# Optimization experiments

Hardware: AMD Instinct MI355X
Metric: run time of the kernel (lower is better)

## Reference

```python
import jax, jax.numpy as jnp
import numpy as np

N = 8192
D = 128
NUM_CLASSES = 1000
MARGIN = 1.0
EPS = 1e-6  # torch.nn.functional.pairwise_distance default eps
FMAX = float(np.finfo(np.float32).max)


def setup_inputs() -> dict:
    key = jax.random.key(0)
    k_e, k_l = jax.random.split(key)
    embed = jax.random.normal(k_e, (N, D), dtype=jnp.float32)
    labels = jax.random.randint(k_l, (N,), 0, NUM_CLASSES, dtype=jnp.int64)
    return {"embed": embed, "labels": labels}


def reference(embed, labels):
    # Pairwise squared-L2 distance matrix: ||xi||^2 - 2 xi.xj + ||xj||^2  -> [N, N]
    norm_sq = jnp.sum(embed * embed, axis=1, keepdims=True)  # [N, 1]
    dist = norm_sq - 2.0 * (embed @ embed.T) + norm_sq.T     # [N, N]

    # Label similarity mask (int in original; float here for the multiplies)
    sim = (labels[:, None] == labels[None, :]).astype(dist.dtype)  # [N, N]

    # Hardest positive: argmax of masked distances
    hardest_pos = jnp.argmax(dist * sim, axis=1)  # [N]

    # Hardest negative: argmin over negatives, sentinel-replacing masked-out entries
    neg_masked = dist * (1.0 - sim)
    hardest_neg = jnp.argmin(neg_masked + (neg_masked <= 0).astype(dist.dtype) * FMAX, axis=1)

    a = embed
    p = embed[hardest_pos]  # [N, D]
    n = embed[hardest_neg]  # [N, D]

    # torch.nn.TripletMarginLoss(margin=MARGIN): mean(relu(d(a,p) - d(a,n) + margin))
    # with d(x, y) = ||x - y + eps||_2 (torch pairwise_distance semantics)
    d_ap = jnp.sqrt(jnp.sum((a - p + EPS) ** 2, axis=1))
    d_an = jnp.sqrt(jnp.sum((a - n + EPS) ** 2, axis=1))
    loss = jnp.mean(jnp.maximum(d_ap - d_an + MARGIN, 0.0))
    return loss
```

## Files before the change

kernel.cpp:

```cpp
#include <hip/hip_runtime.h>
#include <cstdint>

typedef unsigned long long u64;
typedef _Float16 half8 __attribute__((ext_vector_type(8)));
typedef float f32x4 __attribute__((ext_vector_type(4)));

static constexpr int Dd = 128;
static constexpr float EPSf = 1e-6f;
static constexpr float MARGINf = 1.0f;
static constexpr float BIGf = 3.0e38f;

__device__ __forceinline__ unsigned fkey(float f) {
  unsigned b = __float_as_uint(f);
  return (b & 0x80000000u) ? ~b : (b | 0x80000000u);
}

__global__ __launch_bounds__(256) void k_prep(const float* __restrict__ E,
                                              _Float16* __restrict__ Ehp,
                                              float* __restrict__ normf) {
  __shared__ float part[4][16];
  const int t = threadIdx.x;
  const int b = blockIdx.x;
  const int ks = t >> 6, r15 = t & 15;
  const int lg = (t >> 4) & 3;
  const float* src = E + (size_t)(b * 16 + r15) * Dd + ks * 32 + lg * 8;
  float4 v0 = *(const float4*)src;
  float4 v1 = *(const float4*)(src + 4);
  half8 hv;
  hv[0] = (_Float16)v0.x; hv[1] = (_Float16)v0.y;
  hv[2] = (_Float16)v0.z; hv[3] = (_Float16)v0.w;
  hv[4] = (_Float16)v1.x; hv[5] = (_Float16)v1.y;
  hv[6] = (_Float16)v1.z; hv[7] = (_Float16)v1.w;
  *(half8*)((char*)Ehp + (size_t)b * 4096 + t * 16) = hv;
  float s = v0.x * v0.x + v0.y * v0.y + v0.z * v0.z + v0.w * v0.w +
            v1.x * v1.x + v1.y * v1.y + v1.z * v1.z + v1.w * v1.w;
  s += __shfl_xor(s, 16);
  s += __shfl_xor(s, 32);
  if (((t >> 4) & 3) == 0) part[ks][r15] = s;
  __syncthreads();
  if (t < 16) normf[b * 16 + t] = part[0][t] + part[1][t] + part[2][t] + part[3][t];
}

__global__ __launch_bounds__(256, 2) void k_gemm(const _Float16* __restrict__ Ehp,
                                                 const float* __restrict__ normf,
                                                 const int* __restrict__ lab,
                                                 u64* __restrict__ posPart,
                                                 u64* __restrict__ negPart) {
  __shared__ __align__(16) char Jb[2][32768];
  __shared__ __align__(16) float njs[1024];
  __shared__ __align__(16) int ljs[1024];

  const int t = threadIdx.x;
  const int w = t >> 6, l = t & 63;
  const int lane15 = l & 15, lg = l >> 4;
  const int iw = w & 1, jw = w >> 1;
  const int panel = blockIdx.x;
  const int strip = blockIdx.y;
  const int ibase = panel * 128;
  const int jbase = strip * 1024;
  const char* jsrc = (const char*)Ehp + (size_t)(jbase >> 4) * 4096;

  #pragma unroll
  for (int q = 0; q < 8; ++q)
    *(half8*)(Jb[0] + q * 4096 + t * 16) = *(const half8*)(jsrc + q * 4096 + t * 16);
  *(float4*)&njs[t * 4] = *(const float4*)&normf[jbase + t * 4];
  *(int4*)&ljs[t * 4] = *(const int4*)&lab[jbase + t * 4];

  const int gi0 = ibase + iw * 64;
  half8 bf[4][4];
  #pragma unroll
  for (int it = 0; it < 4; ++it)
    #pragma unroll
    for (int ks = 0; ks < 4; ++ks)
      bf[it][ks] = *(const half8*)(Ehp + ((size_t)((gi0 >> 4) + it) * 4 + ks) * 512 +
                                   (size_t)l * 8);
  int li[4];
  #pragma unroll
  for (int it = 0; it < 4; ++it) li[it] = lab[gi0 + it * 16 + lane15];
  __syncthreads();

  float bp[4] = {-BIGf, -BIGf, -BIGf, -BIGf};
  float bn[4] = {BIGf, BIGf, BIGf, BIGf};

  for (int tile = 0; tile < 8; ++tile) {
    const int cur = tile & 1;
    half8 sreg[8];
    if (tile < 7) {
      const char* s = jsrc + (size_t)(tile + 1) * 32768;
      #pragma unroll
      for (int q = 0; q < 8; ++q) sreg[q] = *(const half8*)(s + q * 4096 + t * 16);
    }

    f32x4 acc[4][4];
    #pragma unroll
    for (int a = 0; a < 4; ++a)
      #pragma unroll
      for (int b = 0; b < 4; ++b) acc[a][b] = (f32x4){0.f, 0.f, 0.f, 0.f};

    #pragma unroll
    for (int ks = 0; ks < 4; ++ks) {
      half8 aj[4];
      #pragma unroll
      for (int jt = 0; jt < 4; ++jt)
        aj[jt] = *(const half8*)(Jb[cur] + ((jw * 4 + jt) * 4 + ks) * 1024 + l * 16);
      __builtin_amdgcn_s_setprio(1);
      #pragma unroll
      for (int jt = 0; jt < 4; ++jt)
        #pragma unroll
        for (int it = 0; it < 4; ++it)
          acc[jt][it] = __builtin_amdgcn_mfma_f32_16x16x32_f16(aj[jt], bf[it][ks], acc[jt][it], 0, 0, 0);
      __builtin_amdgcn_s_setprio(0);
    }

    #pragma unroll
    for (int jt = 0; jt < 4; ++jt) {
      const int jr0 = tile * 128 + jw * 64 + jt * 16 + lg * 4;
      const float4 nj4 = *(const float4*)&njs[jr0];
      const int4 lj4 = *(const int4*)&ljs[jr0];
      #pragma unroll
      for (int it = 0; it < 4; ++it) {
        float c0 = fmaf(acc[jt][it][0], -2.0f, nj4.x);
        float c1 = fmaf(acc[jt][it][1], -2.0f, nj4.y);
        float c2 = fmaf(acc[jt][it][2], -2.0f, nj4.z);
        float c3 = fmaf(acc[jt][it][3], -2.0f, nj4.w);
        c0 = __uint_as_float((__float_as_uint(c0) & 0xFFFFFC00u) | (unsigned)(jr0 + 0));
        c1 = __uint_as_float((__float_as_uint(c1) & 0xFFFFFC00u) | (unsigned)(jr0 + 1));
        c2 = __uint_as_float((__float_as_uint(c2) & 0xFFFFFC00u) | (unsigned)(jr0 + 2));
        c3 = __uint_as_float((__float_as_uint(c3) & 0xFFFFFC00u) | (unsigned)(jr0 + 3));
        bool s0 = (lj4.x == li[it]), s1 = (lj4.y == li[it]);
        bool s2 = (lj4.z == li[it]), s3 = (lj4.w == li[it]);
        float p0 = s0 ? c0 : -BIGf, p1 = s1 ? c1 : -BIGf;
        float p2 = s2 ? c2 : -BIGf, p3 = s3 ? c3 : -BIGf;
        float n0 = s0 ? BIGf : c0, n1 = s1 ? BIGf : c1;
        float n2 = s2 ? BIGf : c2, n3 = s3 ? BIGf : c3;
        bp[it] = fmaxf(bp[it], fmaxf(fmaxf(p0, p1), fmaxf(p2, p3)));
        bn[it] = fminf(bn[it], fminf(fminf(n0, n1), fminf(n2, n3)));
      }
    }

    if (tile < 7) {
      #pragma unroll
      for (int q = 0; q < 8; ++q)
        *(half8*)(Jb[cur ^ 1] + q * 4096 + t * 16) = sreg[q];
    }
    __syncthreads();
  }

  #pragma unroll
  for (int it = 0; it < 4; ++it) {
    bp[it] = fmaxf(bp[it], __shfl_xor(bp[it], 16));
    bp[it] = fmaxf(bp[it], __shfl_xor(bp[it], 32));
    bn[it] = fminf(bn[it], __shfl_xor(bn[it], 16));
    bn[it] = fminf(bn[it], __shfl_xor(bn[it], 32));
  }
  if (l < 16) {
    const int slot = strip * 2 + jw;
    #pragma unroll
    for (int it = 0; it < 4; ++it) {
      int gi = ibase + iw * 64 + it * 16 + lane15;
      unsigned gjp = (unsigned)jbase + (__float_as_uint(bp[it]) & 1023u);
      unsigned gjn = (unsigned)jbase + (__float_as_uint(bn[it]) & 1023u);
      posPart[(size_t)slot * 8192 + gi] =
          ((u64)fkey(bp[it]) << 32) | (u64)(0xFFFFFFFFu - gjp);
      negPart[(size_t)slot * 8192 + gi] = ((u64)fkey(bn[it]) << 32) | (u64)gjn;
    }
  }
}

__global__ __launch_bounds__(256) void k_final(const float* __restrict__ E,
                                               const u64* __restrict__ posPart,
                                               const u64* __restrict__ negPart,
                                               float* __restrict__ rowLoss) {
  int i = (blockIdx.x * 256 + threadIdx.x) >> 6;
  int l = threadIdx.x & 63;
  u64 pp = 0ull, np = ~0ull;
  if (l < 16) {
    pp = posPart[(size_t)l * 8192 + i];
    np = negPart[(size_t)l * 8192 + i];
  }
  #pragma unroll
  for (int off = 1; off < 64; off <<= 1) {
    u64 a = __shfl_xor(pp, off);
    u64 b = __shfl_xor(np, off);
    pp = pp > a ? pp : a;
    np = np < b ? np : b;
  }
  int jp = (int)((0xFFFFFFFFu - (unsigned)(pp & 0xFFFFFFFFull)) & 8191u);
  int jn = (int)((unsigned)(np & 0xFFFFFFFFull) & 8191u);
  float2 a = *(const float2*)(E + (size_t)i * Dd + l * 2);
  float2 p = *(const float2*)(E + (size_t)jp * Dd + l * 2);
  float2 n = *(const float2*)(E + (size_t)jn * Dd + l * 2);
  float dx = a.x - p.x + EPSf, dy = a.y - p.y + EPSf;
  float sap = dx * dx + dy * dy;
  dx = a.x - n.x + EPSf;
  dy = a.y - n.y + EPSf;
  float san = dx * dx + dy * dy;
  #pragma unroll
  for (int off = 32; off; off >>= 1) {
    sap += __shfl_xor(sap, off);
    san += __shfl_xor(san, off);
  }
  if (l == 0) rowLoss[i] = fmaxf(sqrtf(sap) - sqrtf(san) + MARGINf, 0.0f);
}

__global__ __launch_bounds__(256) void k_reduce(const float* __restrict__ rowLoss,
                                                float* __restrict__ out) {
  __shared__ float s[256];
  int t = threadIdx.x;
  float sum = 0.f;
  for (int q = 0; q < 32; ++q) sum += rowLoss[t + 256 * q];
  s[t] = sum;
  __syncthreads();
  for (int off = 128; off; off >>= 1) {
    if (t < off) s[t] += s[t + off];
    __syncthreads();
  }
  if (t == 0) out[0] = s[0] * (1.0f / 8192.0f);
}

extern "C" void kernel_launch(void* const* d_in, const int* in_sizes, int n_in,
                              void* d_out, int out_size, void* d_ws, size_t ws_size,
                              hipStream_t stream) {
  const float* E = (const float*)d_in[0];
  const int* lab = (const int*)d_in[1];
  float* out = (float*)d_out;

  char* wsp = (char*)d_ws;
  u64* posPart = (u64*)wsp;
  u64* negPart = (u64*)(wsp + (1024 << 10));
  float* normf = (float*)(wsp + (2048 << 10));
  float* rowLoss = (float*)(wsp + (2080 << 10));
  _Float16* Ehp = (_Float16*)(wsp + (2112 << 10));

  k_prep<<<512, 256, 0, stream>>>(E, Ehp, normf);
  k_gemm<<<dim3(64, 8), 256, 0, stream>>>(Ehp, normf, lab, posPart, negPart);
  k_final<<<2048, 256, 0, stream>>>(E, posPart, negPart, rowLoss);
  k_reduce<<<1, 256, 0, stream>>>(rowLoss, out);
}
```

Measured before the change: 44.92 us.

## Drop LDS staging in distance GEMM; load J fragments directly from global memory

The GEMM kernel no longer stages J-tiles, norms and labels through double-buffered shared memory with barriers. Each wave now streams its own 256-column J slice straight from global memory (L2) into MFMA operand registers, and the grid doubles to 16 column strips. The reduction kernel combines 32 partial slots instead of 16. This removes LDS traffic and __syncthreads stalls and raises parallelism, at the cost of more global/L2 reads, no data reuse across waves, and fewer low mantissa bits left to carry the index.

New measurement: 44.05 us. About the same (-2.0%).

```diff
diff --git a/kernel.cpp b/kernel.cpp
--- a/kernel.cpp
+++ b/kernel.cpp
@@ -46,104 +46,69 @@
                                                  const int* __restrict__ lab,
                                                  u64* __restrict__ posPart,
                                                  u64* __restrict__ negPart) {
-  __shared__ __align__(16) char Jb[2][32768];
-  __shared__ __align__(16) float njs[1024];
-  __shared__ __align__(16) int ljs[1024];
-
   const int t = threadIdx.x;
   const int w = t >> 6, l = t & 63;
   const int lane15 = l & 15, lg = l >> 4;
-  const int iw = w & 1, jw = w >> 1;
-  const int panel = blockIdx.x;
-  const int strip = blockIdx.y;
-  const int ibase = panel * 128;
-  const int jbase = strip * 1024;
-  const char* jsrc = (const char*)Ehp + (size_t)(jbase >> 4) * 4096;
-
-  #pragma unroll
-  for (int q = 0; q < 8; ++q)
-    *(half8*)(Jb[0] + q * 4096 + t * 16) = *(const half8*)(jsrc + q * 4096 + t * 16);
-  *(float4*)&njs[t * 4] = *(const float4*)&normf[jbase + t * 4];
-  *(int4*)&ljs[t * 4] = *(const int4*)&lab[jbase + t * 4];
-
-  const int gi0 = ibase + iw * 64;
+  const int iw = w & 1, jh = w >> 1;
+  const int ibase = blockIdx.x * 128 + iw * 64;
+  const int slot = blockIdx.y * 2 + jh;
+  const int jbase = slot * 256;
+
   half8 bf[4][4];
   #pragma unroll
   for (int it = 0; it < 4; ++it)
     #pragma unroll
     for (int ks = 0; ks < 4; ++ks)
-      bf[it][ks] = *(const half8*)(Ehp + ((size_t)((gi0 >> 4) + it) * 4 + ks) * 512 +
+      bf[it][ks] = *(const half8*)(Ehp + ((size_t)((ibase >> 4) + it) * 4 + ks) * 512 +
                                    (size_t)l * 8);
   int li[4];
   #pragma unroll
-  for (int it = 0; it < 4; ++it) li[it] = lab[gi0 + it * 16 + lane15];
-  __syncthreads();
+  for (int it = 0; it < 4; ++it) li[it] = lab[ibase + it * 16 + lane15];
 
   float bp[4] = {-BIGf, -BIGf, -BIGf, -BIGf};
   float bn[4] = {BIGf, BIGf, BIGf, BIGf};
 
-  for (int tile = 0; tile < 8; ++tile) {
-    const int cur = tile & 1;
-    half8 sreg[8];
-    if (tile < 7) {
-      const char* s = jsrc + (size_t)(tile + 1) * 32768;
+  #pragma unroll
+  for (int chunk = 0; chunk < 16; ++chunk) {
+    const size_t jt16 = (size_t)(jbase >> 4) + chunk;
+    half8 aj[4];
+    #pragma unroll
+    for (int ks = 0; ks < 4; ++ks)
+      aj[ks] = *(const half8*)(Ehp + (jt16 * 4 + ks) * 512 + (size_t)l * 8);
+    const int jr0 = chunk * 16 + lg * 4;
+    const float4 nj4 = *(const float4*)(normf + jbase + jr0);
+    const int4 lj4 = *(const int4*)(lab + jbase + jr0);
+
+    f32x4 acc[4];
+    #pragma unroll
+    for (int it = 0; it < 4; ++it) acc[it] = (f32x4){0.f, 0.f, 0.f, 0.f};
+    __builtin_amdgcn_s_setprio(1);
+    #pragma unroll
+    for (int ks = 0; ks < 4; ++ks)
       #pragma unroll
-      for (int q = 0; q < 8; ++q) sreg[q] = *(const half8*)(s + q * 4096 + t * 16);
+      for (int it = 0; it < 4; ++it)
+        acc[it] = __builtin_amdgcn_mfma_f32_16x16x32_f16(aj[ks], bf[it][ks], acc[it], 0, 0, 0);
+    __builtin_amdgcn_s_setprio(0);
+
+    #pragma unroll
+    for (int it = 0; it < 4; ++it) {
+      float c0 = fmaf(acc[it][0], -2.0f, nj4.x);
+      float c1 = fmaf(acc[it][1], -2.0f, nj4.y);
+      float c2 = fmaf(acc[it][2], -2.0f, nj4.z);
+      float c3 = fmaf(acc[it][3], -2.0f, nj4.w);
+      c0 = __uint_as_float((__float_as_uint(c0) & 0xFFFFFF00u) | (unsigned)(jr0 + 0));
+      c1 = __uint_as_float((__float_as_uint(c1) & 0xFFFFFF00u) | (unsigned)(jr0 + 1));
+      c2 = __uint_as_float((__float_as_uint(c2) & 0xFFFFFF00u) | (unsigned)(jr0 + 2));
+      c3 = __uint_as_float((__float_as_uint(c3) & 0xFFFFFF00u) | (unsigned)(jr0 + 3));
+      bool s0 = (lj4.x == li[it]), s1 = (lj4.y == li[it]);
+      bool s2 = (lj4.z == li[it]), s3 = (lj4.w == li[it]);
+      float p0 = s0 ? c0 : -BIGf, p1 = s1 ? c1 : -BIGf;
+      float p2 = s2 ? c2 : -BIGf, p3 = s3 ? c3 : -BIGf;
+      float n0 = s0 ? BIGf : c0, n1 = s1 ? BIGf : c1;
+      float n2 = s2 ? BIGf : c2, n3 = s3 ? BIGf : c3;
+      bp[it] = fmaxf(bp[it], fmaxf(fmaxf(p0, p1), fmaxf(p2, p3)));
+      bn[it] = fminf(bn[it], fminf(fminf(n0, n1), fminf(n2, n3)));
     }
-
-    f32x4 acc[4][4];
-    #pragma unroll
-    for (int a = 0; a < 4; ++a)
-      #pragma unroll
-      for (int b = 0; b < 4; ++b) acc[a][b] = (f32x4){0.f, 0.f, 0.f, 0.f};
-
-    #pragma unroll
-    for (int ks = 0; ks < 4; ++ks) {
-      half8 aj[4];
-      #pragma unroll
-      for (int jt = 0; jt < 4; ++jt)
-        aj[jt] = *(const half8*)(Jb[cur] + ((jw * 4 + jt) * 4 + ks) * 1024 + l * 16);
-      __builtin_amdgcn_s_setprio(1);
-      #pragma unroll
-      for (int jt = 0; jt < 4; ++jt)
-        #pragma unroll
-        for (int it = 0; it < 4; ++it)
-          acc[jt][it] = __builtin_amdgcn_mfma_f32_16x16x32_f16(aj[jt], bf[it][ks], acc[jt][it], 0, 0, 0);
-      __builtin_amdgcn_s_setprio(0);
-    }
-
-    #pragma unroll
-    for (int jt = 0; jt < 4; ++jt) {
-      const int jr0 = tile * 128 + jw * 64 + jt * 16 + lg * 4;
-      const float4 nj4 = *(const float4*)&njs[jr0];
-      const int4 lj4 = *(const int4*)&ljs[jr0];
-      #pragma unroll
-      for (int it = 0; it < 4; ++it) {
-        float c0 = fmaf(acc[jt][it][0], -2.0f, nj4.x);
-        float c1 = fmaf(acc[jt][it][1], -2.0f, nj4.y);
-        float c2 = fmaf(acc[jt][it][2], -2.0f, nj4.z);
-        float c3 = fmaf(acc[jt][it][3], -2.0f, nj4.w);
-        c0 = __uint_as_float((__float_as_uint(c0) & 0xFFFFFC00u) | (unsigned)(jr0 + 0));
-        c1 = __uint_as_float((__float_as_uint(c1) & 0xFFFFFC00u) | (unsigned)(jr0 + 1));
-        c2 = __uint_as_float((__float_as_uint(c2) & 0xFFFFFC00u) | (unsigned)(jr0 + 2));
-        c3 = __uint_as_float((__float_as_uint(c3) & 0xFFFFFC00u) | (unsigned)(jr0 + 3));
-        bool s0 = (lj4.x == li[it]), s1 = (lj4.y == li[it]);
-        bool s2 = (lj4.z == li[it]), s3 = (lj4.w == li[it]);
-        float p0 = s0 ? c0 : -BIGf, p1 = s1 ? c1 : -BIGf;
-        float p2 = s2 ? c2 : -BIGf, p3 = s3 ? c3 : -BIGf;
-        float n0 = s0 ? BIGf : c0, n1 = s1 ? BIGf : c1;
-        float n2 = s2 ? BIGf : c2, n3 = s3 ? BIGf : c3;
-        bp[it] = fmaxf(bp[it], fmaxf(fmaxf(p0, p1), fmaxf(p2, p3)));
-        bn[it] = fminf(bn[it], fminf(fminf(n0, n1), fminf(n2, n3)));
-      }
-    }
-
-    if (tile < 7) {
-      #pragma unroll
-      for (int q = 0; q < 8; ++q)
-        *(half8*)(Jb[cur ^ 1] + q * 4096 + t * 16) = sreg[q];
-    }
-    __syncthreads();
   }
 
   #pragma unroll
@@ -154,12 +119,11 @@
     bn[it] = fminf(bn[it], __shfl_xor(bn[it], 32));
   }
   if (l < 16) {
-    const int slot = strip * 2 + jw;
     #pragma unroll
     for (int it = 0; it < 4; ++it) {
-      int gi = ibase + iw * 64 + it * 16 + lane15;
-      unsigned gjp = (unsigned)jbase + (__float_as_uint(bp[it]) & 1023u);
-      unsigned gjn = (unsigned)jbase + (__float_as_uint(bn[it]) & 1023u);
+      int gi = ibase + it * 16 + lane15;
+      unsigned gjp = (unsigned)jbase + (__float_as_uint(bp[it]) & 255u);
+      unsigned gjn = (unsigned)jbase + (__float_as_uint(bn[it]) & 255u);
       posPart[(size_t)slot * 8192 + gi] =
           ((u64)fkey(bp[it]) << 32) | (u64)(0xFFFFFFFFu - gjp);
       negPart[(size_t)slot * 8192 + gi] = ((u64)fkey(bn[it]) << 32) | (u64)gjn;
@@ -174,7 +138,7 @@
   int i = (blockIdx.x * 256 + threadIdx.x) >> 6;
   int l = threadIdx.x & 63;
   u64 pp = 0ull, np = ~0ull;
-  if (l < 16) {
+  if (l < 32) {
     pp = posPart[(size_t)l * 8192 + i];
     np = negPart[(size_t)l * 8192 + i];
   }
@@ -227,13 +191,13 @@
 
   char* wsp = (char*)d_ws;
   u64* posPart = (u64*)wsp;
-  u64* negPart = (u64*)(wsp + (1024 << 10));
-  float* normf = (float*)(wsp + (2048 << 10));
-  float* rowLoss = (float*)(wsp + (2080 << 10));
-  _Float16* Ehp = (_Float16*)(wsp + (2112 << 10));
+  u64* negPart = (u64*)(wsp + (2048 << 10));
+  float* normf = (float*)(wsp + (4096 << 10));
+  float* rowLoss = (float*)(wsp + (4128 << 10));
+  _Float16* Ehp = (_Float16*)(wsp + (4160 << 10));
 
   k_prep<<<512, 256, 0, stream>>>(E, Ehp, normf);
-  k_gemm<<<dim3(64, 8), 256, 0, stream>>>(Ehp, normf, lab, posPart, negPart);
+  k_gemm<<<dim3(64, 16), 256, 0, stream>>>(Ehp, normf, lab, posPart, negPart);
   k_final<<<2048, 256, 0, stream>>>(E, posPart, negPart, rowLoss);
   k_reduce<<<1, 256, 0, stream>>>(rowLoss, out);
 }
```
